# Optimization experiments

Measured on AMD Instinct MI355X. Metric: run time of the kernel, lower is better.

Reference implementation:

```python
import jax, jax.numpy as jnp
from jax import lax
import numpy as np

H_MAX = 0.05  # Euler max step size, from ode_solve


def setup_inputs() -> dict:
    key = jax.random.key(0)
    k1, k2, k3 = jax.random.split(key, 3)
    B, D, H, T = 8192, 64, 128, 41
    z0 = jax.random.normal(k1, (B, D), dtype=jnp.float32)
    # uniform time grid, spacing 0.1 -> 2 Euler sub-steps per interval
    t = jnp.arange(T, dtype=jnp.float32) * 0.1
    # small init so the explicit-Euler trajectory stays bounded
    W1 = jax.random.normal(k2, (D, H), dtype=jnp.float32) * 0.05
    b1 = jnp.zeros((H,), dtype=jnp.float32)
    W2 = jax.random.normal(k3, (H, D), dtype=jnp.float32) * 0.05
    b2 = jnp.zeros((D,), dtype=jnp.float32)
    return {"z0": z0, "t": t, "W1": W1, "b1": b1, "W2": W2, "b2": b2}


def reference(z0, t, W1, b1, W2, b2):
    # Dynamics net f(z, t): 2-layer tanh MLP (time-invariant VaeODEF instance)
    def f(z, tt):
        return jnp.tanh(z @ W1 + b1) @ W2 + b2

    # n_steps derived host-side from the (uniform) grid spacing, mirroring the
    # original .item() sync: n_steps = ceil(|t1 - t0| / h_max)
    t_np = np.asarray(t)
    n_steps = int(np.ceil(abs(t_np[1] - t_np[0]) / H_MAX))

    def interval(z, t01):
        t0, t1 = t01
        h = (t1 - t0) / n_steps

        def sub(carry, _):
            z, tc = carry
            return (z + h * f(z, tc), tc + h), None

        (z, _), _ = lax.scan(sub, (z, t0), None, length=n_steps)
        return z, None

    # scan over the time_len-1 intervals (the outer Python loop in forward)
    zT, _ = lax.scan(interval, z0, (t[:-1], t[1:]))
    # return_whole_sequence=False default -> z[-1]
    return zT
```

## Files before the change

### kernel.cpp

```cpp
#include <hip/hip_runtime.h>
#include <hip/hip_bf16.h>

typedef float          f32x4  __attribute__((ext_vector_type(4)));
typedef short          bf16x8 __attribute__((ext_vector_type(8)));
typedef unsigned short u16x4  __attribute__((ext_vector_type(4)));

#define Bsz  8192
#define Dsz  64
#define Hsz  128
#define Tsz  41
#define ROWS 16
#define NT   256

#define MFMA(a,b,c) __builtin_amdgcn_mfma_f32_16x16x32_bf16((a),(b),(c),0,0,0)

__device__ __forceinline__ float fast_tanh(float x) {
    float ax = __builtin_fabsf(x);
    float e  = __expf(-2.0f * ax);
    float r  = (1.0f - e) * __builtin_amdgcn_rcpf(1.0f + e);
    return __builtin_copysignf(r, x);
}

__device__ __forceinline__ unsigned short bf2u(__hip_bfloat16 h) {
    union { __hip_bfloat16 b; unsigned short u; } v; v.b = h; return v.u;
}

union FragU { bf16x8 f; unsigned short h[8]; };

__device__ __forceinline__ bf16x8 pack8(const float* x) {
    FragU H;
    #pragma unroll
    for (int i = 0; i < 8; ++i) H.h[i] = bf2u(__float2bfloat16(x[i]));
    return H.f;
}

__device__ __forceinline__ u16x4 packq(const f32x4& x) {
    u16x4 H;
    #pragma unroll
    for (int i = 0; i < 4; ++i) H[i] = bf2u(__float2bfloat16(x[i]));
    return H;
}

__device__ __forceinline__ bf16x8 ldb128(const unsigned short* base, int byteoff) {
    return *(const bf16x8*)((const char*)base + byteoff);
}
__device__ __forceinline__ void stb64(unsigned short* base, int byteoff, u16x4 v) {
    *(u16x4*)((char*)base + byteoff) = v;
}

__global__ __launch_bounds__(NT, 2)
void ode_mfma17(const float* __restrict__ z0, const float* __restrict__ t,
                const float* __restrict__ W1, const float* __restrict__ b1,
                const float* __restrict__ W2, const float* __restrict__ b2,
                float* __restrict__ out)
{
    __shared__ __align__(16) unsigned short zHs[ROWS * Dsz];
    __shared__ __align__(16) unsigned short aHs[ROWS * Hsz];
    __shared__ float ts[Tsz];

    const int tid  = threadIdx.x;
    const int lane = tid & 63;
    const int w    = tid >> 6;
    const int g    = lane >> 4;
    const int c    = lane & 15;
    const int r0   = blockIdx.x * ROWS;

    if (tid < Tsz) ts[tid] = t[tid];

    f32x4 zreg = *(const f32x4*)&z0[(r0 + c) * Dsz + 16*w + 4*g];

    bf16x8 w1t[2][2];
    #pragma unroll
    for (int nt = 0; nt < 2; ++nt) {
        const int n = 32*w + 16*nt + c;
        #pragma unroll
        for (int kt = 0; kt < 2; ++kt) {
            float tmp[8];
            #pragma unroll
            for (int i = 0; i < 8; ++i) tmp[i] = W1[(32*kt + 8*g + i) * Hsz + n];
            w1t[nt][kt] = pack8(tmp);
        }
    }
    bf16x8 w2t[4];
    {
        const int n = 16*w + c;
        #pragma unroll
        for (int kt2 = 0; kt2 < 4; ++kt2) {
            float tmp[8];
            #pragma unroll
            for (int i = 0; i < 8; ++i) tmp[i] = W2[(32*kt2 + 8*g + i) * Dsz + n];
            w2t[kt2] = pack8(tmp);
        }
    }
    f32x4 b1v[2], b2v;
    #pragma unroll
    for (int nt = 0; nt < 2; ++nt)
        #pragma unroll
        for (int reg = 0; reg < 4; ++reg)
            b1v[nt][reg] = b1[16*(2*w + nt) + 4*g + reg];
    #pragma unroll
    for (int reg = 0; reg < 4; ++reg) b2v[reg] = b2[16*w + 4*g + reg];

    const int zw = (c*128 + (16*w + 4*g)*2) ^ ((c & 7) << 4);
    int zrd[2], aw[2], ard[4];
    #pragma unroll
    for (int kt = 0; kt < 2; ++kt)
        zrd[kt] = (c*128 + (32*kt + 8*g)*2) ^ ((c & 7) << 4);
    #pragma unroll
    for (int nt = 0; nt < 2; ++nt)
        aw[nt] = (c*256 + (32*w + 16*nt + 4*g)*2) ^ ((c & 7) << 4);
    #pragma unroll
    for (int kt2 = 0; kt2 < 4; ++kt2)
        ard[kt2] = (c*256 + (32*kt2 + 8*g)*2) ^ ((c & 7) << 4);

    auto z_to_lds = [&]() {
        stb64(zHs, zw, packq(zreg));
    };

    z_to_lds();
    __syncthreads();

    const int n_steps = (int)ceilf(fabsf(ts[1] - ts[0]) / 0.05f);

    for (int iv = 0; iv < Tsz - 1; ++iv) {
        const float h = (ts[iv + 1] - ts[iv]) / (float)n_steps;
        for (int s = 0; s < n_steps; ++s) {
            bf16x8 zh0 = ldb128(zHs, zrd[0]), zh1 = ldb128(zHs, zrd[1]);
            #pragma unroll
            for (int nt = 0; nt < 2; ++nt) {
                f32x4 aA = b1v[nt];
                aA = MFMA(w1t[nt][0], zh0, aA);
                aA = MFMA(w1t[nt][1], zh1, aA);
                f32x4 tv;
                #pragma unroll
                for (int reg = 0; reg < 4; ++reg) tv[reg] = fast_tanh(aA[reg]);
                stb64(aHs, aw[nt], packq(tv));
            }
            __syncthreads();
            bf16x8 ah0 = ldb128(aHs, ard[0]), ah1 = ldb128(aHs, ard[1]);
            bf16x8 ah2 = ldb128(aHs, ard[2]), ah3 = ldb128(aHs, ard[3]);
            f32x4 dA = b2v;
            f32x4 dB = {0,0,0,0};
            dA = MFMA(w2t[0], ah0, dA);
            dB = MFMA(w2t[1], ah1, dB);
            dA = MFMA(w2t[2], ah2, dA);
            dB = MFMA(w2t[3], ah3, dB);
            f32x4 dz = dA + dB;
            zreg += h * dz;
            z_to_lds();
            __syncthreads();
        }
    }

    *(f32x4*)&out[(r0 + c) * Dsz + 16*w + 4*g] = zreg;
}

extern "C" void kernel_launch(void* const* d_in, const int* in_sizes, int n_in,
                              void* d_out, int out_size, void* d_ws, size_t ws_size,
                              hipStream_t stream) {
    const float* z0 = (const float*)d_in[0];
    const float* t  = (const float*)d_in[1];
    const float* W1 = (const float*)d_in[2];
    const float* b1 = (const float*)d_in[3];
    const float* W2 = (const float*)d_in[4];
    const float* b2 = (const float*)d_in[5];
    float* out = (float*)d_out;
    (void)in_sizes; (void)n_in; (void)out_size; (void)d_ws; (void)ws_size;

    ode_mfma17<<<dim3(Bsz / ROWS), dim3(NT), 0, stream>>>(z0, t, W1, b1, W2, b2, out);
}
```

Measured before the change: 57.71 us.

## Replicate second-layer GEMM per wave to drop one barrier per Euler step

Each wave now computes the full 64-wide dz for its 16 rows using all of W2 in registers, and keeps a private copy of z in its own LDS slice. The second __syncthreads per sub-step goes away, and the hidden-activation buffer is double-buffered so a fast wave cannot overwrite data another wave is still reading. The cost is four times the second-layer MFMA work (16 instead of 4 MFMAs per wave per step) and more registers for W2 fragments and z state, which may hurt occupancy under the 2-block launch bound.

```diff
diff --git a/kernel.cpp b/kernel.cpp
--- a/kernel.cpp
+++ b/kernel.cpp
@@ -49,13 +49,13 @@
 }
 
 __global__ __launch_bounds__(NT, 2)
-void ode_mfma17(const float* __restrict__ z0, const float* __restrict__ t,
+void ode_mfma18(const float* __restrict__ z0, const float* __restrict__ t,
                 const float* __restrict__ W1, const float* __restrict__ b1,
                 const float* __restrict__ W2, const float* __restrict__ b2,
                 float* __restrict__ out)
 {
-    __shared__ __align__(16) unsigned short zHs[ROWS * Dsz];
-    __shared__ __align__(16) unsigned short aHs[ROWS * Hsz];
+    __shared__ __align__(16) unsigned short aHs[2][ROWS * Hsz];
+    __shared__ __align__(16) unsigned short zscr[4 * ROWS * Dsz];
     __shared__ float ts[Tsz];
 
     const int tid  = threadIdx.x;
@@ -67,7 +67,10 @@
 
     if (tid < Tsz) ts[tid] = t[tid];
 
-    f32x4 zreg = *(const f32x4*)&z0[(r0 + c) * Dsz + 16*w + 4*g];
+    f32x4 zf[4];
+    #pragma unroll
+    for (int mt = 0; mt < 4; ++mt)
+        zf[mt] = *(const f32x4*)&z0[(r0 + c) * Dsz + 16*mt + 4*g];
 
     bf16x8 w1t[2][2];
     #pragma unroll
@@ -81,31 +84,38 @@
             w1t[nt][kt] = pack8(tmp);
         }
     }
-    bf16x8 w2t[4];
-    {
-        const int n = 16*w + c;
+    bf16x8 w2t[4][4];
+    #pragma unroll
+    for (int mt = 0; mt < 4; ++mt) {
+        const int n = 16*mt + c;
         #pragma unroll
         for (int kt2 = 0; kt2 < 4; ++kt2) {
             float tmp[8];
             #pragma unroll
             for (int i = 0; i < 8; ++i) tmp[i] = W2[(32*kt2 + 8*g + i) * Dsz + n];
-            w2t[kt2] = pack8(tmp);
+            w2t[mt][kt2] = pack8(tmp);
         }
     }
-    f32x4 b1v[2], b2v;
+    f32x4 b1v[2], b2v[4];
     #pragma unroll
     for (int nt = 0; nt < 2; ++nt)
         #pragma unroll
         for (int reg = 0; reg < 4; ++reg)
             b1v[nt][reg] = b1[16*(2*w + nt) + 4*g + reg];
     #pragma unroll
-    for (int reg = 0; reg < 4; ++reg) b2v[reg] = b2[16*w + 4*g + reg];
+    for (int mt = 0; mt < 4; ++mt)
+        #pragma unroll
+        for (int reg = 0; reg < 4; ++reg)
+            b2v[mt][reg] = b2[16*mt + 4*g + reg];
 
-    const int zw = (c*128 + (16*w + 4*g)*2) ^ ((c & 7) << 4);
-    int zrd[2], aw[2], ard[4];
+    const int zbase = w * (ROWS * Dsz * 2);
+    int zw[4], zrd[2], aw[2], ard[4];
+    #pragma unroll
+    for (int mt = 0; mt < 4; ++mt)
+        zw[mt] = zbase + ((c*128 + (16*mt + 4*g)*2) ^ ((c & 7) << 4));
     #pragma unroll
     for (int kt = 0; kt < 2; ++kt)
-        zrd[kt] = (c*128 + (32*kt + 8*g)*2) ^ ((c & 7) << 4);
+        zrd[kt] = zbase + ((c*128 + (32*kt + 8*g)*2) ^ ((c & 7) << 4));
     #pragma unroll
     for (int nt = 0; nt < 2; ++nt)
         aw[nt] = (c*256 + (32*w + 16*nt + 4*g)*2) ^ ((c & 7) << 4);
@@ -113,46 +123,48 @@
     for (int kt2 = 0; kt2 < 4; ++kt2)
         ard[kt2] = (c*256 + (32*kt2 + 8*g)*2) ^ ((c & 7) << 4);
 
-    auto z_to_lds = [&]() {
-        stb64(zHs, zw, packq(zreg));
-    };
-
-    z_to_lds();
+    #pragma unroll
+    for (int mt = 0; mt < 4; ++mt) stb64(zscr, zw[mt], packq(zf[mt]));
     __syncthreads();
 
     const int n_steps = (int)ceilf(fabsf(ts[1] - ts[0]) / 0.05f);
 
+    int cur = 0;
     for (int iv = 0; iv < Tsz - 1; ++iv) {
         const float h = (ts[iv + 1] - ts[iv]) / (float)n_steps;
         for (int s = 0; s < n_steps; ++s) {
-            bf16x8 zh0 = ldb128(zHs, zrd[0]), zh1 = ldb128(zHs, zrd[1]);
+            bf16x8 zb0 = ldb128(zscr, zrd[0]), zb1 = ldb128(zscr, zrd[1]);
+            unsigned short* aH = aHs[cur];
             #pragma unroll
             for (int nt = 0; nt < 2; ++nt) {
                 f32x4 aA = b1v[nt];
-                aA = MFMA(w1t[nt][0], zh0, aA);
-                aA = MFMA(w1t[nt][1], zh1, aA);
+                aA = MFMA(w1t[nt][0], zb0, aA);
+                aA = MFMA(w1t[nt][1], zb1, aA);
                 f32x4 tv;
                 #pragma unroll
                 for (int reg = 0; reg < 4; ++reg) tv[reg] = fast_tanh(aA[reg]);
-                stb64(aHs, aw[nt], packq(tv));
+                stb64(aH, aw[nt], packq(tv));
             }
             __syncthreads();
-            bf16x8 ah0 = ldb128(aHs, ard[0]), ah1 = ldb128(aHs, ard[1]);
-            bf16x8 ah2 = ldb128(aHs, ard[2]), ah3 = ldb128(aHs, ard[3]);
-            f32x4 dA = b2v;
-            f32x4 dB = {0,0,0,0};
-            dA = MFMA(w2t[0], ah0, dA);
-            dB = MFMA(w2t[1], ah1, dB);
-            dA = MFMA(w2t[2], ah2, dA);
-            dB = MFMA(w2t[3], ah3, dB);
-            f32x4 dz = dA + dB;
-            zreg += h * dz;
-            z_to_lds();
-            __syncthreads();
+            bf16x8 ah0 = ldb128(aH, ard[0]), ah1 = ldb128(aH, ard[1]);
+            bf16x8 ah2 = ldb128(aH, ard[2]), ah3 = ldb128(aH, ard[3]);
+            #pragma unroll
+            for (int mt = 0; mt < 4; ++mt) {
+                f32x4 dA = b2v[mt];
+                dA = MFMA(w2t[mt][0], ah0, dA);
+                dA = MFMA(w2t[mt][1], ah1, dA);
+                dA = MFMA(w2t[mt][2], ah2, dA);
+                dA = MFMA(w2t[mt][3], ah3, dA);
+                zf[mt] += h * dA;
+                stb64(zscr, zw[mt], packq(zf[mt]));
+            }
+            cur ^= 1;
         }
     }
 
-    *(f32x4*)&out[(r0 + c) * Dsz + 16*w + 4*g] = zreg;
+    #pragma unroll
+    for (int mt = 0; mt < 4; ++mt)
+        *(f32x4*)&out[(r0 + c) * Dsz + 16*mt + 4*g] = zf[mt];
 }
 
 extern "C" void kernel_launch(void* const* d_in, const int* in_sizes, int n_in,
@@ -167,5 +179,5 @@
     float* out = (float*)d_out;
     (void)in_sizes; (void)n_in; (void)out_size; (void)d_ws; (void)ws_size;
 
-    ode_mfma17<<<dim3(Bsz / ROWS), dim3(NT), 0, stream>>>(z0, t, W1, b1, W2, b2, out);
+    ode_mfma18<<<dim3(Bsz / ROWS), dim3(NT), 0, stream>>>(z0, t, W1, b1, W2, b2, out);
 }
```

Result: slower. 74.80 us (+29.6%).
